# Performance work log

Measured on AMD Instinct MI355X. Metric: run time of the kernel, lower is better.

Reference implementation:

```python
import jax, jax.numpy as jnp
import numpy as np

IN_CH, OUT_CH, KS = 64, 128, 3
GRID, DEG = 8, 3
STRIDE, PAD = 1, 1
SIZE = IN_CH * KS * KS            # 576
NCOEF = GRID + DEG                # 11
GRID_RANGE = (-1.0, 1.0)


def _xavier_uniform(key, shape):
    fan_out, fan_in = shape
    a = float(np.sqrt(6.0 / (fan_in + fan_out)))
    return jax.random.uniform(key, shape, minval=-a, maxval=a, dtype=jnp.float32)


def setup_inputs() -> dict:
    key = jax.random.key(0)
    k1, k2, k3 = jax.random.split(key, 3)
    x = jax.random.normal(k1, (8, IN_CH, 32, 32), dtype=jnp.float32)
    # non-trainable knot grid, one row per unfolded feature
    knots = jnp.tile(jnp.linspace(GRID_RANGE[0], GRID_RANGE[1], GRID + 1, dtype=jnp.float32)[None, :], (SIZE, 1))
    coeff = 0.1 * jax.random.normal(k2, (OUT_CH, SIZE, NCOEF), dtype=jnp.float32)
    base_weights = _xavier_uniform(k3, (OUT_CH, SIZE))
    spline_weights = jnp.ones((OUT_CH, SIZE), dtype=jnp.float32)
    return {"x": x, "knots": knots, "coeff": coeff,
            "base_weights": base_weights, "spline_weights": spline_weights}


def bspline_basis(x, grid, k):
    # x: (S, P) evaluation points; grid: (S, G+1) knots. Returns (S, G+k, P).
    h = (grid[:, -1:] - grid[:, :1]) / (grid.shape[1] - 1)
    left = grid[:, :1] - h * jnp.arange(k, 0, -1, dtype=x.dtype)
    right = grid[:, -1:] + h * jnp.arange(1, k + 1, dtype=x.dtype)
    g = jnp.concatenate([left, grid, right], axis=1)  # (S, G+1+2k)
    xe = x[:, None, :]
    B = ((xe >= g[:, :-1, None]) & (xe < g[:, 1:, None])).astype(x.dtype)
    for d in range(1, k + 1):  # de Boor recursion over fixed degree
        B = ((xe - g[:, :-(d + 1), None]) / (g[:, d:-1, None] - g[:, :-(d + 1), None]) * B[:, :-1]
             + (g[:, d + 1:, None] - xe) / (g[:, d + 1:, None] - g[:, 1:-d, None]) * B[:, 1:])
    return B


def _unfold(x):
    # torch F.unfold with channel-major (c, kh, kw) feature ordering
    N, C, H, W = x.shape
    xp = jnp.pad(x, ((0, 0), (0, 0), (PAD, PAD), (PAD, PAD)))
    Hp = (H + 2 * PAD - KS) // STRIDE + 1
    Wp = (W + 2 * PAD - KS) // STRIDE + 1
    patches = jnp.stack([xp[:, :, i:i + STRIDE * Hp:STRIDE, j:j + STRIDE * Wp:STRIDE]
                         for i in range(KS) for j in range(KS)], axis=2)  # (N, C, KS*KS, Hp, Wp)
    L = Hp * Wp
    u = patches.reshape(N, SIZE, L)              # (N, size, L)
    u = jnp.transpose(u, (1, 0, 2)).reshape(SIZE, N * L)  # (size, N*L), col = n*L + l
    return u, Hp, Wp


def reference(x, knots, coeff, base_weights, spline_weights):
    N = x.shape[0]
    u, Hp, Wp = _unfold(x)                                   # (size, P)
    base = base_weights @ jax.nn.silu(u)                     # (Cout, P)
    B = bspline_basis(u, knots, DEG)                         # (size, ncoef, P)
    eff = spline_weights[:, :, None] * coeff                 # (Cout, size, ncoef)
    spl = jnp.einsum('csj,sjp->cp', eff, B)                  # (Cout, P)
    out = (base + spl).reshape(OUT_CH, N, Hp, Wp)
    return jnp.transpose(out, (1, 0, 2, 3))                  # (N, Cout, Hp, Wp)
```

## Files before the change

kernel.cpp:

```cpp
#include <hip/hip_runtime.h>


typedef __attribute__((ext_vector_type(8))) short bf16x8;
typedef __attribute__((ext_vector_type(4))) float f32x4;
typedef __attribute__((ext_vector_type(16))) float f32x16;
typedef __attribute__((ext_vector_type(4))) unsigned short u16x4;

#define WSWZ_BYTES 1769472
#define PHI_OFF    WSWZ_BYTES
#define PHI_BYTES  14205696
#define PART_OFF   (PHI_OFF + PHI_BYTES)

__device__ __forceinline__ short f2bf(float f) {
    union { float f; unsigned u; } c; c.f = f;
    unsigned r = c.u + 0x7fffu + ((c.u >> 16) & 1u);
    return (short)(r >> 16);
}
__device__ __forceinline__ float bf2f(unsigned short u) {
    union { unsigned u; float f; } c; c.u = ((unsigned)u) << 16;
    return c.f;
}

__global__ void kan_prep(const float* __restrict__ coeff,
                         const float* __restrict__ basew,
                         const float* __restrict__ splw,
                         const float* __restrict__ x,
                         short* __restrict__ Wswz,
                         short* __restrict__ Phi) {
    __shared__ float coeffL[6336];
    __shared__ float basewL[576];
    __shared__ float splwL[576];
    __shared__ unsigned short xs[64 * 32];
    const int t = threadIdx.x;

    if (blockIdx.x < 272) {
        const int rowid = blockIdx.x;
        const int n     = rowid / 34;
        const int ypad  = rowid - n * 34;
        const int y     = ypad - 1;
        const bool yvalid = (y >= 0 && y < 32);

        if (yvalid) {
#pragma unroll
            for (int it = 0; it < 2; ++it) {
                int cg = t + it * 256;
                int ci = cg >> 3, q = cg & 7;
                f32x4 v = *(const f32x4*)(x + (((n * 64 + ci) * 32 + y) * 32 + q * 4));
                u16x4 p;
                p.x = (unsigned short)f2bf(v.x); p.y = (unsigned short)f2bf(v.y);
                p.z = (unsigned short)f2bf(v.z); p.w = (unsigned short)f2bf(v.w);
                *(u16x4*)&xs[ci * 32 + q * 4] = p;
            }
        }
        __syncthreads();

        const size_t rowbase = (size_t)rowid * 12 * 2176;
        for (int it = t; it < 272; it += 256) {
            int xp = it >> 3, cch = it & 7, c0 = cch << 3;
            bool interior = yvalid && (xp >= 1 && xp <= 32);
            int px = xp - 1;
            int pxc = px < 0 ? 0 : (px > 31 ? 31 : px);
            bf16x8 packs[12];
#pragma unroll
            for (int j = 0; j < 8; ++j) {
                float v = interior ? bf2f(xs[(c0 + j) * 32 + pxc]) : 0.f;
                float tt = 4.f * v + 7.f;
                int   i0 = -100;
                float b0 = 0.f, b1 = 0.f, b2 = 0.f, b3 = 0.f;
                if (tt >= 0.f && tt < 14.f) {
                    i0 = (int)tt;
                    float fr  = tt - (float)i0;
                    float omf = 1.f - fr;
                    float fr2 = fr * fr, fr3 = fr2 * fr;
                    b0 = omf * omf * omf * (1.f / 6.f);
                    b1 = (3.f * fr3 - 6.f * fr2 + 4.f) * (1.f / 6.f);
                    b2 = (-3.f * fr3 + 3.f * fr2 + 3.f * fr + 1.f) * (1.f / 6.f);
                    b3 = fr3 * (1.f / 6.f);
                }
                float silu = v * __builtin_amdgcn_rcpf(1.f + __expf(-v));
                packs[0][j] = f2bf(silu);
#pragma unroll
                for (int f = 1; f < 12; ++f) {
                    int jj = f - 1;
                    float val = 0.f;
                    val = (jj == i0 - 3) ? b0 : val;
                    val = (jj == i0 - 2) ? b1 : val;
                    val = (jj == i0 - 1) ? b2 : val;
                    val = (jj == i0    ) ? b3 : val;
                    packs[f][j] = f2bf(val);
                }
            }
            int swz = (cch ^ (xp & 7)) << 3;
#pragma unroll
            for (int f = 0; f < 12; ++f)
                *(bf16x8*)&Phi[rowbase + (size_t)f * 2176 + xp * 64 + swz] = packs[f];
        }
    } else {
        const int co = blockIdx.x - 272;
        const float* crow = coeff + co * 6336;
        for (int i = t; i < 6336; i += 256) coeffL[i] = crow[i];
        for (int i = t; i < 576; i += 256) {
            basewL[i] = basew[co * 576 + i];
            splwL[i]  = splw[co * 576 + i];
        }
        __syncthreads();
        const int cb = co >> 5, lm = co & 31;
        for (int c = t; c < 864; c += 256) {
            int kk16 = c >> 1, kh = c & 1;
            int f  = kk16 / 36;
            int rm = kk16 - f * 36;
            int tap = rm >> 2, q = rm & 3;
            bf16x8 pack;
#pragma unroll
            for (int j = 0; j < 8; ++j) {
                int ci = q * 16 + kh * 8 + j;
                int s  = ci * 9 + tap;
                float v = (f == 0) ? basewL[s] : splwL[s] * coeffL[s * 11 + (f - 1)];
                pack[j] = f2bf(v);
            }
            *(bf16x8*)(Wswz + (size_t)((kk16 * 4 + cb) * 64 + kh * 32 + lm) * 8) = pack;
        }
    }
}

__global__ __launch_bounds__(256, 4)
void kan_gemm(const short* __restrict__ Phi,
              const short* __restrict__ Wswz,
              float* __restrict__ part) {
    __shared__ short Bs[2 * 8704];

    const int t  = threadIdx.x;
    const int w  = t >> 6;
    const int l  = t & 63;
    const int ln = l & 31;
    const int kh = l >> 5;

    const int fg    = blockIdx.x >> 7;
    const int ptile = blockIdx.x & 127;
    const int n     = ptile >> 4;
    const int y0    = (ptile & 15) << 1;

    const char* phiB = (const char*)Phi;
    const int planeBase = (n * 34 + y0) * 12 + fg * 2;
#pragma unroll
    for (int k = 0; k < 9; ++k) {
        int i = t + k * 256;
        if (i < 2176) {
            int pl  = i / 1088;
            int r2  = i - pl * 1088;
            int row = r2 / 272;
            int m   = r2 - row * 272;
            const char* s = phiB + (size_t)(planeBase + row * 12 + pl) * 4352 + m * 16;
            auto gsrc = (const __attribute__((address_space(1))) unsigned int*)s;
            auto ldst = (__attribute__((address_space(3))) unsigned int*)((char*)&Bs[0] + i * 16);
            __builtin_amdgcn_global_load_lds(gsrc, ldst, 16, 0, 0);
        }
    }
    __syncthreads();

    f32x16 acc[2];
#pragma unroll
    for (int pb = 0; pb < 2; ++pb)
#pragma unroll
        for (int r = 0; r < 16; ++r)
            acc[pb][r] = 0.f;

    const short* Abase = Wswz + (size_t)w * 512 + (size_t)l * 8;
#pragma unroll 1
    for (int p = 0; p < 2; ++p) {
        const short* B0 = Bs + p * 8704;
        const int kbase = (fg * 2 + p) * 36;
#pragma unroll
        for (int q = 0; q < 4; ++q) {
#pragma unroll
            for (int dx = 0; dx < 3; ++dx) {
                bf16x8 a0 = *(const bf16x8*)(Abase + (size_t)(kbase + (0 * 3 + dx) * 4 + q) * 2048);
                bf16x8 a1 = *(const bf16x8*)(Abase + (size_t)(kbase + (1 * 3 + dx) * 4 + q) * 2048);
                bf16x8 a2 = *(const bf16x8*)(Abase + (size_t)(kbase + (2 * 3 + dx) * 4 + q) * 2048);
                const int c   = q * 2 + kh;
                const int key = (ln + dx) & 7;
                bf16x8 b0, b1, b2, b3;
                {
                    int pix0 = 0 * 34 + ln + dx;
                    int pix1 = 1 * 34 + ln + dx;
                    int pix2 = 2 * 34 + ln + dx;
                    int pix3 = 3 * 34 + ln + dx;
                    int slot = (c ^ key) << 3;
                    b0 = *(const bf16x8*)&B0[pix0 * 64 + slot];
                    b1 = *(const bf16x8*)&B0[pix1 * 64 + slot];
                    b2 = *(const bf16x8*)&B0[pix2 * 64 + slot];
                    b3 = *(const bf16x8*)&B0[pix3 * 64 + slot];
                }
                acc[0] = __builtin_amdgcn_mfma_f32_32x32x16_bf16(a0, b0, acc[0], 0, 0, 0);
                acc[1] = __builtin_amdgcn_mfma_f32_32x32x16_bf16(a0, b1, acc[1], 0, 0, 0);
                acc[0] = __builtin_amdgcn_mfma_f32_32x32x16_bf16(a1, b1, acc[0], 0, 0, 0);
                acc[1] = __builtin_amdgcn_mfma_f32_32x32x16_bf16(a1, b2, acc[1], 0, 0, 0);
                acc[0] = __builtin_amdgcn_mfma_f32_32x32x16_bf16(a2, b2, acc[0], 0, 0, 0);
                acc[1] = __builtin_amdgcn_mfma_f32_32x32x16_bf16(a2, b3, acc[1], 0, 0, 0);
            }
        }
    }

    float* dst = part + (size_t)fg * 1048576;
#pragma unroll
    for (int pb = 0; pb < 2; ++pb) {
        int y = y0 + pb;
#pragma unroll
        for (int r = 0; r < 16; ++r) {
            int row = (r & 3) + 8 * (r >> 2) + 4 * kh;
            int co  = w * 32 + row;
            dst[((size_t)(n * 128 + co) * 32 + y) * 32 + ln] = acc[pb][r];
        }
    }
}

__global__ void kan_reduce(const float* __restrict__ part,
                           float* __restrict__ out) {
    const int r = blockIdx.x;
    const int p = r & 127;
    const int i = r >> 7;
    const int n  = p >> 4;
    const int yp = p & 15;
    const int c  = i * 256 + threadIdx.x;
    const int co = c >> 4;
    const int rem = c & 15;
    const int yy = rem >> 3, xq = rem & 7;
    const size_t idx = ((size_t)(n * 128 + co) * 32 + yp * 2 + yy) * 8 + xq;
    f32x4 a = ((const f32x4*)part)[idx];
#pragma unroll
    for (int s = 1; s < 6; ++s)
        a += ((const f32x4*)(part + (size_t)s * 1048576))[idx];
    ((f32x4*)out)[idx] = a;
}

extern "C" void kernel_launch(void* const* d_in, const int* in_sizes, int n_in,
                              void* d_out, int out_size, void* d_ws, size_t ws_size,
                              hipStream_t stream) {
    const float* x     = (const float*)d_in[0];
    const float* coeff = (const float*)d_in[2];
    const float* basew = (const float*)d_in[3];
    const float* splw  = (const float*)d_in[4];
    float* out = (float*)d_out;

    short* Wswz = (short*)d_ws;
    short* Phi  = (short*)((char*)d_ws + PHI_OFF);
    float* part = (float*)((char*)d_ws + PART_OFF);

    kan_prep<<<400, 256, 0, stream>>>(coeff, basew, splw, x, Wswz, Phi);
    kan_gemm<<<768, 256, 0, stream>>>(Phi, Wswz, part);
    kan_reduce<<<1024, 256, 0, stream>>>(part, out);
}
```

Baseline: 107.1 us.

## Fuse split-K reduction into GEMM via last-arriving-block atomic counter

Drops the separate reduce kernel. Each GEMM block now bumps a per-tile atomic counter once its partial sums are written, and the sixth block to arrive sums all six partials and writes the output. Counters are zeroed in the prep kernel. It also fully unrolls the outer K-plane loop and raises wave priority around the MFMA section. This saves one kernel launch and its tail, but the last-arriving block per tile must re-read all six partial buffers, and the change depends on correct memory fences.

```diff
diff --git a/kernel.cpp b/kernel.cpp
--- a/kernel.cpp
+++ b/kernel.cpp
@@ -10,6 +10,7 @@
 #define PHI_OFF    WSWZ_BYTES
 #define PHI_BYTES  14205696
 #define PART_OFF   (PHI_OFF + PHI_BYTES)
+#define FLAGS_OFF  (PART_OFF + 6 * 4194304)
 
 __device__ __forceinline__ short f2bf(float f) {
     union { float f; unsigned u; } c; c.f = f;
@@ -26,7 +27,8 @@
                          const float* __restrict__ splw,
                          const float* __restrict__ x,
                          short* __restrict__ Wswz,
-                         short* __restrict__ Phi) {
+                         short* __restrict__ Phi,
+                         unsigned int* __restrict__ flags) {
     __shared__ float coeffL[6336];
     __shared__ float basewL[576];
     __shared__ float splwL[576];
@@ -97,6 +99,7 @@
         }
     } else {
         const int co = blockIdx.x - 272;
+        if (blockIdx.x == 399 && t < 128) flags[t] = 0;
         const float* crow = coeff + co * 6336;
         for (int i = t; i < 6336; i += 256) coeffL[i] = crow[i];
         for (int i = t; i < 576; i += 256) {
@@ -126,8 +129,11 @@
 __global__ __launch_bounds__(256, 4)
 void kan_gemm(const short* __restrict__ Phi,
               const short* __restrict__ Wswz,
-              float* __restrict__ part) {
+              float* __restrict__ part,
+              unsigned int* __restrict__ flags,
+              float* __restrict__ out) {
     __shared__ short Bs[2 * 8704];
+    __shared__ int lastFlag;
 
     const int t  = threadIdx.x;
     const int w  = t >> 6;
@@ -166,7 +172,8 @@
             acc[pb][r] = 0.f;
 
     const short* Abase = Wswz + (size_t)w * 512 + (size_t)l * 8;
-#pragma unroll 1
+    __builtin_amdgcn_s_setprio(1);
+#pragma unroll
     for (int p = 0; p < 2; ++p) {
         const short* B0 = Bs + p * 8704;
         const int kbase = (fg * 2 + p) * 36;
@@ -200,6 +207,7 @@
             }
         }
     }
+    __builtin_amdgcn_s_setprio(0);
 
     float* dst = part + (size_t)fg * 1048576;
 #pragma unroll
@@ -212,25 +220,30 @@
             dst[((size_t)(n * 128 + co) * 32 + y) * 32 + ln] = acc[pb][r];
         }
     }
-}
-
-__global__ void kan_reduce(const float* __restrict__ part,
-                           float* __restrict__ out) {
-    const int r = blockIdx.x;
-    const int p = r & 127;
-    const int i = r >> 7;
-    const int n  = p >> 4;
-    const int yp = p & 15;
-    const int c  = i * 256 + threadIdx.x;
-    const int co = c >> 4;
-    const int rem = c & 15;
-    const int yy = rem >> 3, xq = rem & 7;
-    const size_t idx = ((size_t)(n * 128 + co) * 32 + yp * 2 + yy) * 8 + xq;
-    f32x4 a = ((const f32x4*)part)[idx];
-#pragma unroll
-    for (int s = 1; s < 6; ++s)
-        a += ((const f32x4*)(part + (size_t)s * 1048576))[idx];
-    ((f32x4*)out)[idx] = a;
+
+    __threadfence();
+    __syncthreads();
+    if (t == 0) {
+        unsigned old = atomicAdd(&flags[ptile], 1u);
+        lastFlag = (old == 5u);
+    }
+    __syncthreads();
+    if (lastFlag) {
+        __threadfence();
+#pragma unroll
+        for (int k = 0; k < 8; ++k) {
+            int c   = t + k * 256;
+            int co  = c >> 4;
+            int rem = c & 15;
+            int yy  = rem >> 3, xq = rem & 7;
+            size_t idx = ((size_t)(n * 128 + co) * 32 + y0 + yy) * 8 + xq;
+            f32x4 a = ((const f32x4*)part)[idx];
+#pragma unroll
+            for (int s = 1; s < 6; ++s)
+                a += ((const f32x4*)(part + (size_t)s * 1048576))[idx];
+            ((f32x4*)out)[idx] = a;
+        }
+    }
 }
 
 extern "C" void kernel_launch(void* const* d_in, const int* in_sizes, int n_in,
@@ -245,8 +258,8 @@
     short* Wswz = (short*)d_ws;
     short* Phi  = (short*)((char*)d_ws + PHI_OFF);
     float* part = (float*)((char*)d_ws + PART_OFF);
-
-    kan_prep<<<400, 256, 0, stream>>>(coeff, basew, splw, x, Wswz, Phi);
-    kan_gemm<<<768, 256, 0, stream>>>(Phi, Wswz, part);
-    kan_reduce<<<1024, 256, 0, stream>>>(part, out);
-}
+    unsigned int* flags = (unsigned int*)((char*)d_ws + FLAGS_OFF);
+
+    kan_prep<<<400, 256, 0, stream>>>(coeff, basew, splw, x, Wswz, Phi, flags);
+    kan_gemm<<<768, 256, 0, stream>>>(Phi, Wswz, part, flags, out);
+}
```

Measured after the change: 209.0 us. 1.95x slower.

## Widen GEMM pixel tile to four output rows per block for weight reuse

Applied to the files above, without the earlier changes.

Each kan_gemm block now computes four output rows instead of two, staging six halo rows of Phi into LDS and running four accumulators per wave. Every weight fragment loaded from global memory now feeds twice as many MFMAs, which halves weight traffic per output and cuts the grid to 384 blocks. The cost is more LDS and registers per block (launch bounds lowered to 2 waves per SIMD) and fewer blocks than CUs on a 256-CU part, so load balance and latency hiding may suffer. The reduce kernel's indexing is remapped to match the new tiling.

```diff
diff --git a/kernel.cpp b/kernel.cpp
--- a/kernel.cpp
+++ b/kernel.cpp
@@ -123,11 +123,11 @@
     }
 }
 
-__global__ __launch_bounds__(256, 4)
+__global__ __launch_bounds__(256, 2)
 void kan_gemm(const short* __restrict__ Phi,
               const short* __restrict__ Wswz,
               float* __restrict__ part) {
-    __shared__ short Bs[2 * 8704];
+    __shared__ short Bs[2 * 6 * 2176];
 
     const int t  = threadIdx.x;
     const int w  = t >> 6;
@@ -135,19 +135,19 @@
     const int ln = l & 31;
     const int kh = l >> 5;
 
-    const int fg    = blockIdx.x >> 7;
-    const int ptile = blockIdx.x & 127;
-    const int n     = ptile >> 4;
-    const int y0    = (ptile & 15) << 1;
+    const int fg     = blockIdx.x >> 6;
+    const int ptile4 = blockIdx.x & 63;
+    const int n      = ptile4 >> 3;
+    const int y0     = (ptile4 & 7) << 2;
 
     const char* phiB = (const char*)Phi;
     const int planeBase = (n * 34 + y0) * 12 + fg * 2;
 #pragma unroll
-    for (int k = 0; k < 9; ++k) {
+    for (int k = 0; k < 13; ++k) {
         int i = t + k * 256;
-        if (i < 2176) {
-            int pl  = i / 1088;
-            int r2  = i - pl * 1088;
+        if (i < 3264) {
+            int pl  = i / 1632;
+            int r2  = i - pl * 1632;
             int row = r2 / 272;
             int m   = r2 - row * 272;
             const char* s = phiB + (size_t)(planeBase + row * 12 + pl) * 4352 + m * 16;
@@ -158,9 +158,9 @@
     }
     __syncthreads();
 
-    f32x16 acc[2];
-#pragma unroll
-    for (int pb = 0; pb < 2; ++pb)
+    f32x16 acc[4];
+#pragma unroll
+    for (int pb = 0; pb < 4; ++pb)
 #pragma unroll
         for (int r = 0; r < 16; ++r)
             acc[pb][r] = 0.f;
@@ -168,7 +168,7 @@
     const short* Abase = Wswz + (size_t)w * 512 + (size_t)l * 8;
 #pragma unroll 1
     for (int p = 0; p < 2; ++p) {
-        const short* B0 = Bs + p * 8704;
+        const short* B0 = Bs + p * 13056;
         const int kbase = (fg * 2 + p) * 36;
 #pragma unroll
         for (int q = 0; q < 4; ++q) {
@@ -179,31 +179,32 @@
                 bf16x8 a2 = *(const bf16x8*)(Abase + (size_t)(kbase + (2 * 3 + dx) * 4 + q) * 2048);
                 const int c   = q * 2 + kh;
                 const int key = (ln + dx) & 7;
-                bf16x8 b0, b1, b2, b3;
-                {
-                    int pix0 = 0 * 34 + ln + dx;
-                    int pix1 = 1 * 34 + ln + dx;
-                    int pix2 = 2 * 34 + ln + dx;
-                    int pix3 = 3 * 34 + ln + dx;
-                    int slot = (c ^ key) << 3;
-                    b0 = *(const bf16x8*)&B0[pix0 * 64 + slot];
-                    b1 = *(const bf16x8*)&B0[pix1 * 64 + slot];
-                    b2 = *(const bf16x8*)&B0[pix2 * 64 + slot];
-                    b3 = *(const bf16x8*)&B0[pix3 * 64 + slot];
-                }
+                const int off = (ln + dx) * 64 + ((c ^ key) << 3);
+                bf16x8 b0 = *(const bf16x8*)&B0[0 * 2176 + off];
+                bf16x8 b1 = *(const bf16x8*)&B0[1 * 2176 + off];
+                bf16x8 b2 = *(const bf16x8*)&B0[2 * 2176 + off];
+                bf16x8 b3 = *(const bf16x8*)&B0[3 * 2176 + off];
+                bf16x8 b4 = *(const bf16x8*)&B0[4 * 2176 + off];
+                bf16x8 b5 = *(const bf16x8*)&B0[5 * 2176 + off];
                 acc[0] = __builtin_amdgcn_mfma_f32_32x32x16_bf16(a0, b0, acc[0], 0, 0, 0);
                 acc[1] = __builtin_amdgcn_mfma_f32_32x32x16_bf16(a0, b1, acc[1], 0, 0, 0);
+                acc[2] = __builtin_amdgcn_mfma_f32_32x32x16_bf16(a0, b2, acc[2], 0, 0, 0);
+                acc[3] = __builtin_amdgcn_mfma_f32_32x32x16_bf16(a0, b3, acc[3], 0, 0, 0);
                 acc[0] = __builtin_amdgcn_mfma_f32_32x32x16_bf16(a1, b1, acc[0], 0, 0, 0);
                 acc[1] = __builtin_amdgcn_mfma_f32_32x32x16_bf16(a1, b2, acc[1], 0, 0, 0);
+                acc[2] = __builtin_amdgcn_mfma_f32_32x32x16_bf16(a1, b3, acc[2], 0, 0, 0);
+                acc[3] = __builtin_amdgcn_mfma_f32_32x32x16_bf16(a1, b4, acc[3], 0, 0, 0);
                 acc[0] = __builtin_amdgcn_mfma_f32_32x32x16_bf16(a2, b2, acc[0], 0, 0, 0);
                 acc[1] = __builtin_amdgcn_mfma_f32_32x32x16_bf16(a2, b3, acc[1], 0, 0, 0);
+                acc[2] = __builtin_amdgcn_mfma_f32_32x32x16_bf16(a2, b4, acc[2], 0, 0, 0);
+                acc[3] = __builtin_amdgcn_mfma_f32_32x32x16_bf16(a2, b5, acc[3], 0, 0, 0);
             }
         }
     }
 
     float* dst = part + (size_t)fg * 1048576;
 #pragma unroll
-    for (int pb = 0; pb < 2; ++pb) {
+    for (int pb = 0; pb < 4; ++pb) {
         int y = y0 + pb;
 #pragma unroll
         for (int r = 0; r < 16; ++r) {
@@ -216,16 +217,16 @@
 
 __global__ void kan_reduce(const float* __restrict__ part,
                            float* __restrict__ out) {
-    const int r = blockIdx.x;
-    const int p = r & 127;
-    const int i = r >> 7;
-    const int n  = p >> 4;
-    const int yp = p & 15;
+    const int r  = blockIdx.x;
+    const int p4 = r & 63;
+    const int i  = r >> 6;
+    const int n  = p4 >> 3;
+    const int ys = p4 & 7;
     const int c  = i * 256 + threadIdx.x;
-    const int co = c >> 4;
-    const int rem = c & 15;
+    const int co = c >> 5;
+    const int rem = c & 31;
     const int yy = rem >> 3, xq = rem & 7;
-    const size_t idx = ((size_t)(n * 128 + co) * 32 + yp * 2 + yy) * 8 + xq;
+    const size_t idx = ((size_t)(n * 128 + co) * 32 + ys * 4 + yy) * 8 + xq;
     f32x4 a = ((const f32x4*)part)[idx];
 #pragma unroll
     for (int s = 1; s < 6; ++s)
@@ -247,6 +248,6 @@
     float* part = (float*)((char*)d_ws + PART_OFF);
 
     kan_prep<<<400, 256, 0, stream>>>(coeff, basew, splw, x, Wswz, Phi);
-    kan_gemm<<<768, 256, 0, stream>>>(Phi, Wswz, part);
+    kan_gemm<<<384, 256, 0, stream>>>(Phi, Wswz, part);
     kan_reduce<<<1024, 256, 0, stream>>>(part, out);
 }
```

New measurement: 108.0 us. No clear change (+0.8%).

## Double-buffer weight tiles in LDS via async global-to-LDS loads in GEMM

Applied to the files above, without the earlier changes.

The GEMM kernel now stages each phase's weight fragments into a double-buffered LDS array with global_load_lds, prefetching the next phase while MFMAs run on the current one. Before, weights were read straight from global memory into registers. The fully unrolled q/dx loops become a rolled 24-phase loop with a barrier each iteration, and launch bounds drop from 4 to 2 blocks per SM to make room for the added LDS. Partial-sum writes and the reduce kernel's loads and stores switch to nontemporal hints. The extra barriers and lower occupancy may cost more than the hidden load latency saves.

```diff
diff --git a/kernel.cpp b/kernel.cpp
--- a/kernel.cpp
+++ b/kernel.cpp
@@ -123,11 +123,12 @@
     }
 }
 
-__global__ __launch_bounds__(256, 4)
+__global__ __launch_bounds__(256, 2)
 void kan_gemm(const short* __restrict__ Phi,
               const short* __restrict__ Wswz,
               float* __restrict__ part) {
     __shared__ short Bs[2 * 8704];
+    __shared__ short As[2][6144];
 
     const int t  = threadIdx.x;
     const int w  = t >> 6;
@@ -151,11 +152,35 @@
             int row = r2 / 272;
             int m   = r2 - row * 272;
             const char* s = phiB + (size_t)(planeBase + row * 12 + pl) * 4352 + m * 16;
-            auto gsrc = (const __attribute__((address_space(1))) unsigned int*)s;
-            auto ldst = (__attribute__((address_space(3))) unsigned int*)((char*)&Bs[0] + i * 16);
-            __builtin_amdgcn_global_load_lds(gsrc, ldst, 16, 0, 0);
-        }
-    }
+            __builtin_amdgcn_global_load_lds(
+                (const __attribute__((address_space(1))) unsigned int*)s,
+                (__attribute__((address_space(3))) unsigned int*)((char*)Bs + i * 16),
+                16, 0, 0);
+        }
+    }
+
+    const char* wB = (const char*)Wswz;
+    auto stageA = [&](int ph, int buf) {
+        int p  = ph / 12;
+        int r3 = ph - p * 12;
+        int q  = r3 / 3;
+        int dx = r3 - q * 3;
+        int kbase = (fg * 2 + p) * 36;
+#pragma unroll
+        for (int k = 0; k < 3; ++k) {
+            int i  = t + k * 256;
+            int dy = i >> 8;
+            int inner = i & 255;
+            int kk = kbase + (dy * 3 + dx) * 4 + q;
+            const char* s = wB + (size_t)kk * 4096 + inner * 16;
+            __builtin_amdgcn_global_load_lds(
+                (const __attribute__((address_space(1))) unsigned int*)s,
+                (__attribute__((address_space(3))) unsigned int*)((char*)&As[buf][0] + i * 16),
+                16, 0, 0);
+        }
+    };
+
+    stageA(0, 0);
     __syncthreads();
 
     f32x16 acc[2];
@@ -165,40 +190,40 @@
         for (int r = 0; r < 16; ++r)
             acc[pb][r] = 0.f;
 
-    const short* Abase = Wswz + (size_t)w * 512 + (size_t)l * 8;
+    int buf = 0;
 #pragma unroll 1
-    for (int p = 0; p < 2; ++p) {
+    for (int ph = 0; ph < 24; ++ph) {
+        if (ph < 23) stageA(ph + 1, buf ^ 1);
+
+        int p  = ph / 12;
+        int r3 = ph - p * 12;
+        int q  = r3 / 3;
+        int dx = r3 - q * 3;
+
+        const char* A0 = (const char*)&As[buf][0];
+        bf16x8 a0 = *(const bf16x8*)(A0 + (0 * 4 + w) * 1024 + l * 16);
+        bf16x8 a1 = *(const bf16x8*)(A0 + (1 * 4 + w) * 1024 + l * 16);
+        bf16x8 a2 = *(const bf16x8*)(A0 + (2 * 4 + w) * 1024 + l * 16);
+
         const short* B0 = Bs + p * 8704;
-        const int kbase = (fg * 2 + p) * 36;
-#pragma unroll
-        for (int q = 0; q < 4; ++q) {
-#pragma unroll
-            for (int dx = 0; dx < 3; ++dx) {
-                bf16x8 a0 = *(const bf16x8*)(Abase + (size_t)(kbase + (0 * 3 + dx) * 4 + q) * 2048);
-                bf16x8 a1 = *(const bf16x8*)(Abase + (size_t)(kbase + (1 * 3 + dx) * 4 + q) * 2048);
-                bf16x8 a2 = *(const bf16x8*)(Abase + (size_t)(kbase + (2 * 3 + dx) * 4 + q) * 2048);
-                const int c   = q * 2 + kh;
-                const int key = (ln + dx) & 7;
-                bf16x8 b0, b1, b2, b3;
-                {
-                    int pix0 = 0 * 34 + ln + dx;
-                    int pix1 = 1 * 34 + ln + dx;
-                    int pix2 = 2 * 34 + ln + dx;
-                    int pix3 = 3 * 34 + ln + dx;
-                    int slot = (c ^ key) << 3;
-                    b0 = *(const bf16x8*)&B0[pix0 * 64 + slot];
-                    b1 = *(const bf16x8*)&B0[pix1 * 64 + slot];
-                    b2 = *(const bf16x8*)&B0[pix2 * 64 + slot];
-                    b3 = *(const bf16x8*)&B0[pix3 * 64 + slot];
-                }
-                acc[0] = __builtin_amdgcn_mfma_f32_32x32x16_bf16(a0, b0, acc[0], 0, 0, 0);
-                acc[1] = __builtin_amdgcn_mfma_f32_32x32x16_bf16(a0, b1, acc[1], 0, 0, 0);
-                acc[0] = __builtin_amdgcn_mfma_f32_32x32x16_bf16(a1, b1, acc[0], 0, 0, 0);
-                acc[1] = __builtin_amdgcn_mfma_f32_32x32x16_bf16(a1, b2, acc[1], 0, 0, 0);
-                acc[0] = __builtin_amdgcn_mfma_f32_32x32x16_bf16(a2, b2, acc[0], 0, 0, 0);
-                acc[1] = __builtin_amdgcn_mfma_f32_32x32x16_bf16(a2, b3, acc[1], 0, 0, 0);
-            }
-        }
+        const int c   = q * 2 + kh;
+        const int key = (ln + dx) & 7;
+        const int slot = (c ^ key) << 3;
+        const int colb = (ln + dx) * 64 + slot;
+        bf16x8 b0 = *(const bf16x8*)&B0[0 * 2176 + colb];
+        bf16x8 b1 = *(const bf16x8*)&B0[1 * 2176 + colb];
+        bf16x8 b2 = *(const bf16x8*)&B0[2 * 2176 + colb];
+        bf16x8 b3 = *(const bf16x8*)&B0[3 * 2176 + colb];
+
+        acc[0] = __builtin_amdgcn_mfma_f32_32x32x16_bf16(a0, b0, acc[0], 0, 0, 0);
+        acc[1] = __builtin_amdgcn_mfma_f32_32x32x16_bf16(a0, b1, acc[1], 0, 0, 0);
+        acc[0] = __builtin_amdgcn_mfma_f32_32x32x16_bf16(a1, b1, acc[0], 0, 0, 0);
+        acc[1] = __builtin_amdgcn_mfma_f32_32x32x16_bf16(a1, b2, acc[1], 0, 0, 0);
+        acc[0] = __builtin_amdgcn_mfma_f32_32x32x16_bf16(a2, b2, acc[0], 0, 0, 0);
+        acc[1] = __builtin_amdgcn_mfma_f32_32x32x16_bf16(a2, b3, acc[1], 0, 0, 0);
+
+        __syncthreads();
+        buf ^= 1;
     }
 
     float* dst = part + (size_t)fg * 1048576;
@@ -209,7 +234,8 @@
         for (int r = 0; r < 16; ++r) {
             int row = (r & 3) + 8 * (r >> 2) + 4 * kh;
             int co  = w * 32 + row;
-            dst[((size_t)(n * 128 + co) * 32 + y) * 32 + ln] = acc[pb][r];
+            __builtin_nontemporal_store(acc[pb][r],
+                &dst[((size_t)(n * 128 + co) * 32 + y) * 32 + ln]);
         }
     }
 }
@@ -226,11 +252,11 @@
     const int rem = c & 15;
     const int yy = rem >> 3, xq = rem & 7;
     const size_t idx = ((size_t)(n * 128 + co) * 32 + yp * 2 + yy) * 8 + xq;
-    f32x4 a = ((const f32x4*)part)[idx];
+    f32x4 a = __builtin_nontemporal_load(&((const f32x4*)part)[idx]);
 #pragma unroll
     for (int s = 1; s < 6; ++s)
-        a += ((const f32x4*)(part + (size_t)s * 1048576))[idx];
-    ((f32x4*)out)[idx] = a;
+        a += __builtin_nontemporal_load(&((const f32x4*)(part + (size_t)s * 1048576))[idx]);
+    __builtin_nontemporal_store(a, &((f32x4*)out)[idx]);
 }
 
 extern "C" void kernel_launch(void* const* d_in, const int* in_sizes, int n_in,
```

Result: slower. 117.4 us (+9.6%).
